# Kernel tuning notes

Hardware: AMD Instinct MI355X
Metric: run time of the kernel (lower is better)

The kernel has to match this reference:

```python
import jax, jax.numpy as jnp
import numpy as np

EPS_MASK = 1e-9   # module fills masked scores with eps, NOT -inf
LN_EPS = 1e-5

def _layer_norm(x, g, b):
    mu = jnp.mean(x, axis=-1, keepdims=True)
    var = jnp.mean(jnp.square(x - mu), axis=-1, keepdims=True)
    return (x - mu) * jax.lax.rsqrt(var + LN_EPS) * g + b

def _mha(q_in, k_in, v_in, wq, bq, wk, bk, wv, bv, wo, bo, mask, nhead):
    B, Sq, D = q_in.shape
    dk = D // nhead
    def proj(x, w, b):
        y = x @ w + b                                   # [B,S,D]
        return y.reshape(B, -1, nhead, dk).transpose(0, 2, 1, 3)  # [B,h,S,dk]
    q, k, v = proj(q_in, wq, bq), proj(k_in, wk, bk), proj(v_in, wv, bv)
    scores = jnp.einsum('bhqd,bhkd->bhqk', q, k) / np.sqrt(dk).astype(q.dtype)
    if mask is not None:
        scores = jnp.where(mask[:, None, :, :] == 0, jnp.asarray(EPS_MASK, scores.dtype), scores)
    p = jax.nn.softmax(scores, axis=-1)                 # dropout = identity (eval)
    x = jnp.einsum('bhqk,bhkd->bhqd', p, v)
    x = x.transpose(0, 2, 1, 3).reshape(B, Sq, D)
    return x @ wo + bo

def _forward_post(tgt, memory, tgt_pos, memory_pos, tgt_mask, memory_mask, p):
    nhead = 8
    # self-attention (q=k=tgt+pos, v=tgt)
    q = tgt + tgt_pos
    sa = _mha(q, q, tgt, p['sa_wq'], p['sa_bq'], p['sa_wk'], p['sa_bk'],
              p['sa_wv'], p['sa_bv'], p['sa_wo'], p['sa_bo'], tgt_mask, nhead)
    tgt = _layer_norm(tgt + sa, p['ln1_g'], p['ln1_b'])
    # cross-attention (q=tgt+tgt_pos, k=memory+memory_pos, v=memory)
    mq = tgt + tgt_pos
    mk = memory + memory_pos
    ca = _mha(mq, mk, memory, p['ca_wq'], p['ca_bq'], p['ca_wk'], p['ca_bk'],
              p['ca_wv'], p['ca_bv'], p['ca_wo'], p['ca_bo'], memory_mask, nhead)
    tgt = _layer_norm(tgt + ca, p['ln2_g'], p['ln2_b'])
    # FFN
    h = jax.nn.relu(tgt @ p['mlp_w1'] + p['mlp_b1'])
    ff = h @ p['mlp_w2'] + p['mlp_b2']
    return _layer_norm(tgt + ff, p['ln3_g'], p['ln3_b'])

def setup_inputs() -> dict:
    key = jax.random.key(0)
    B, S, M, D, H = 4, 1024, 1024, 512, 2048
    ks = iter(jax.random.split(key, 40))
    d = {
        'tgt': jax.random.normal(next(ks), (B, S, D), jnp.float32),
        'memory': jax.random.normal(next(ks), (B, M, D), jnp.float32),
        'tgt_pos': jax.random.normal(next(ks), (B, S, D), jnp.float32),
        'memory_pos': jax.random.normal(next(ks), (B, M, D), jnp.float32),
        'tgt_mask': jax.random.randint(next(ks), (B, S, S), 0, 2, jnp.int32),
        'memory_mask': jax.random.randint(next(ks), (B, S, M), 0, 2, jnp.int32),
    }
    for pre in ('sa', 'ca'):
        for nm in ('q', 'k', 'v', 'o'):
            d[f'{pre}_w{nm}'] = jax.random.normal(next(ks), (D, D), jnp.float32) * 0.02
            d[f'{pre}_b{nm}'] = jnp.zeros((D,), jnp.float32)
    for i in (1, 2, 3):
        d[f'ln{i}_g'] = jnp.ones((D,), jnp.float32)
        d[f'ln{i}_b'] = jnp.zeros((D,), jnp.float32)
    d['mlp_w1'] = jax.random.normal(next(ks), (D, H), jnp.float32) * 0.02
    d['mlp_b1'] = jnp.zeros((H,), jnp.float32)
    d['mlp_w2'] = jax.random.normal(next(ks), (H, D), jnp.float32) * 0.02
    d['mlp_b2'] = jnp.zeros((D,), jnp.float32)
    return d

def reference(tgt, memory, tgt_pos, memory_pos, tgt_mask, memory_mask,
              sa_wq, sa_bq, sa_wk, sa_bk, sa_wv, sa_bv, sa_wo, sa_bo,
              ca_wq, ca_bq, ca_wk, ca_bk, ca_wv, ca_bv, ca_wo, ca_bo,
              ln1_g, ln1_b, ln2_g, ln2_b, ln3_g, ln3_b,
              mlp_w1, mlp_b1, mlp_w2, mlp_b2):
    p = dict(sa_wq=sa_wq, sa_bq=sa_bq, sa_wk=sa_wk, sa_bk=sa_bk, sa_wv=sa_wv,
             sa_bv=sa_bv, sa_wo=sa_wo, sa_bo=sa_bo, ca_wq=ca_wq, ca_bq=ca_bq,
             ca_wk=ca_wk, ca_bk=ca_bk, ca_wv=ca_wv, ca_bv=ca_bv, ca_wo=ca_wo,
             ca_bo=ca_bo, ln1_g=ln1_g, ln1_b=ln1_b, ln2_g=ln2_g, ln2_b=ln2_b,
             ln3_g=ln3_g, ln3_b=ln3_b, mlp_w1=mlp_w1, mlp_b1=mlp_b1,
             mlp_w2=mlp_w2, mlp_b2=mlp_b2)
    return _forward_post(tgt, memory, tgt_pos, memory_pos, tgt_mask, memory_mask, p)
```

## Files before the change

### kernel.cpp

```cpp
#include <hip/hip_runtime.h>
#include <stdint.h>

typedef unsigned int u32;
typedef unsigned long long u64;
typedef unsigned short u16;
typedef __attribute__((ext_vector_type(8))) __bf16 bf16x8;
typedef __attribute__((ext_vector_type(4))) float f32x4;

#define DEV __device__ __forceinline__

DEV u16 f2bf(float f) {
    u32 x = __builtin_bit_cast(u32, f);
    u32 r = (x + 0x7FFFu + ((x >> 16) & 1u)) >> 16;
    return (u16)r;
}

DEV float bf2f(u16 x) {
    u32 u = (u32)x << 16;
    return __builtin_bit_cast(float, u);
}

DEV void unp8(uint4 u, float* f) {
    f[0] = bf2f((u16)u.x); f[1] = bf2f((u16)(u.x >> 16));
    f[2] = bf2f((u16)u.y); f[3] = bf2f((u16)(u.y >> 16));
    f[4] = bf2f((u16)u.z); f[5] = bf2f((u16)(u.z >> 16));
    f[6] = bf2f((u16)u.w); f[7] = bf2f((u16)(u.w >> 16));
}

DEV bf16x8 ldg8(const u16* p) {
    return __builtin_bit_cast(bf16x8, *(const uint4*)p);
}

DEV u32 pk2(float a, float b) {
    return (u32)f2bf(a) | ((u32)f2bf(b) << 16);
}

DEV void g2l16(const u16* g, u16* l) {
    __builtin_amdgcn_global_load_lds(
        (const __attribute__((address_space(1))) u32*)g,
        (__attribute__((address_space(3))) u32*)l, 16, 0, 0);
}

DEV f32x4 mfma16(bf16x8 a, bf16x8 b, f32x4 c) {
    return __builtin_amdgcn_mfma_f32_16x16x32_bf16(a, b, c, 0, 0, 0);
}

struct ProArgs {
    const float* w[10];
    u16* wtbase;
    const float4 *tgt, *tpos, *mem, *mpos;
    ushort4 *qin, *tgtb, *memb, *mkb, *tposb;
    const int4 *m1, *m2;
    u32 *o1, *o2;
};
__global__ __launch_bounds__(256) void prologue_kernel(ProArgs a) {
    const int bx = blockIdx.x, t = threadIdx.x;
    if (bx < 10240) {
        int z = bx >> 10, bxx = bx & 1023;
        int Kd = (z == 9) ? 2048 : 512;
        int Nd = (z == 8) ? 2048 : 512;
        size_t off = (z < 8) ? (size_t)z * 262144
                             : (z == 8 ? (size_t)2097152 : (size_t)3145728);
        u16* out = a.wtbase + off;
        int nx = Nd / 32;
        int txile = bxx % nx, tyile = bxx / nx;
        if (tyile >= Kd / 32) return;
        const float* w = a.w[z];
        __shared__ float tl[32][33];
        int tx = t & 31, ty = t >> 5;
#pragma unroll
        for (int j = 0; j < 4; ++j)
            tl[ty + j * 8][tx] = w[(size_t)(tyile * 32 + ty + j * 8) * Nd + txile * 32 + tx];
        __syncthreads();
#pragma unroll
        for (int j = 0; j < 4; ++j)
            out[(size_t)(txile * 32 + ty + j * 8) * Kd + tyile * 32 + tx] = f2bf(tl[tx][ty + j * 8]);
    } else if (bx < 12288) {
        int i = (bx - 10240) * 256 + t;
        float4 tt = a.tgt[i], p = a.tpos[i], m = a.mem[i], mp = a.mpos[i];
        a.qin[i]  = make_ushort4(f2bf(tt.x + p.x), f2bf(tt.y + p.y), f2bf(tt.z + p.z), f2bf(tt.w + p.w));
        a.tgtb[i] = make_ushort4(f2bf(tt.x), f2bf(tt.y), f2bf(tt.z), f2bf(tt.w));
        a.memb[i] = make_ushort4(f2bf(m.x), f2bf(m.y), f2bf(m.z), f2bf(m.w));
        a.mkb[i]  = make_ushort4(f2bf(m.x + mp.x), f2bf(m.y + mp.y), f2bf(m.z + mp.z), f2bf(m.w + mp.w));
        a.tposb[i]= make_ushort4(f2bf(p.x), f2bf(p.y), f2bf(p.z), f2bf(p.w));
    } else {
        int i = (bx - 12288) * 256 + t;
        const int n8 = 524288;
        bool first = i < n8;
        int idx = first ? i : i - n8;
        const int4* src = first ? a.m1 : a.m2;
        int4 x = src[idx * 2], y = src[idx * 2 + 1];
        u32 by = (u32)(x.x != 0) | ((u32)(x.y != 0) << 1) | ((u32)(x.z != 0) << 2) |
                 ((u32)(x.w != 0) << 3) | ((u32)(y.x != 0) << 4) | ((u32)(y.y != 0) << 5) |
                 ((u32)(y.z != 0) << 6) | ((u32)(y.w != 0) << 7);
        u32 w = by | (__shfl_down(by, 1) << 8) | (__shfl_down(by, 2) << 16) |
                (__shfl_down(by, 3) << 24);
        if ((t & 3) == 0) (first ? a.o1 : a.o2)[idx >> 2] = w;
    }
}

struct GemmSet { const u16* A; const u16* W; const float* bias; void* out; float oscale; int epi; };
struct GemmArgs5 { GemmSet s[5]; };

template <int BM, int BN>
__global__ __launch_bounds__(256) void gemm_kernel(GemmArgs5 args, int M, int N, int Kd) {
    constexpr int MF = BM / 32, NF = BN / 32;
    const GemmSet gs = args.s[blockIdx.z];
    const u16* __restrict__ A = gs.A;
    const u16* __restrict__ W = gs.W;
    const int t = threadIdx.x;
    const int lane = t & 63;
    const int g = lane >> 4, r16 = lane & 15;
    const int wave = t >> 6;
    const int wm = wave >> 1, wn = wave & 1;
    const int nwg = gridDim.x * gridDim.y;
    const int fid = blockIdx.y * gridDim.x + blockIdx.x;
    const int qq = nwg >> 3;
    const int lid = (fid & 7) * qq + (fid >> 3);
    const int m0 = (lid / gridDim.x) * BM, n0 = (lid % gridDim.x) * BN;

    __shared__ __align__(16) u16 As[BM * 64];
    __shared__ __align__(16) u16 Bs[BN * 64];

    f32x4 acc[MF][NF];
#pragma unroll
    for (int m = 0; m < MF; ++m)
#pragma unroll
        for (int n = 0; n < NF; ++n) acc[m][n] = f32x4{0.f, 0.f, 0.f, 0.f};

    for (int kk = 0; kk < Kd; kk += 64) {
        __syncthreads();
#pragma unroll
        for (int i = 0; i < BM / 32; ++i) {
            int cid = t + i * 256, row = cid >> 3, c = cid & 7;
            g2l16(A + (size_t)(m0 + row) * Kd + kk + ((c ^ (row & 7)) << 3), &As[cid << 3]);
        }
#pragma unroll
        for (int i = 0; i < BN / 32; ++i) {
            int cid = t + i * 256, row = cid >> 3, c = cid & 7;
            g2l16(W + (size_t)(n0 + row) * Kd + kk + ((c ^ (row & 7)) << 3), &Bs[cid << 3]);
        }
        __syncthreads();
#pragma unroll
        for (int ks = 0; ks < 2; ++ks) {
            bf16x8 af[MF], bfr[NF];
#pragma unroll
            for (int m = 0; m < MF; ++m) {
                int row = wm * (MF * 16) + m * 16 + r16;
                af[m] = *(const bf16x8*)&As[(row << 6) + (((ks * 4 + g) ^ (row & 7)) << 3)];
            }
#pragma unroll
            for (int n = 0; n < NF; ++n) {
                int row = wn * (NF * 16) + n * 16 + r16;
                bfr[n] = *(const bf16x8*)&Bs[(row << 6) + (((ks * 4 + g) ^ (row & 7)) << 3)];
            }
#pragma unroll
            for (int m = 0; m < MF; ++m)
#pragma unroll
                for (int n = 0; n < NF; ++n)
                    acc[m][n] = mfma16(af[m], bfr[n], acc[m][n]);
        }
    }
    const int epi = gs.epi;
#pragma unroll
    for (int m = 0; m < MF; ++m) {
        int row0 = m0 + wm * (MF * 16) + m * 16 + g * 4;
#pragma unroll
        for (int n = 0; n < NF; ++n) {
            int col = n0 + wn * (NF * 16) + n * 16 + r16;
            float bv = gs.bias[col];
            float v[4];
#pragma unroll
            for (int r = 0; r < 4; ++r) v[r] = (acc[m][n][r] + bv) * gs.oscale;
            if (epi == 1) {
#pragma unroll
                for (int r = 0; r < 4; ++r) v[r] = fmaxf(v[r], 0.f);
            }
            if (epi == 3) {
                int bb = row0 >> 10, s = row0 & 1023;
                u16* o = (u16*)gs.out +
                         ((size_t)(bb * 8 + (col >> 6)) * 64 + (col & 63)) * 1024 + s;
                *(ushort4*)o = make_ushort4(f2bf(v[0]), f2bf(v[1]), f2bf(v[2]), f2bf(v[3]));
            } else {
                u16* o = (u16*)gs.out;
#pragma unroll
                for (int r = 0; r < 4; ++r) o[(size_t)(row0 + r) * N + col] = f2bf(v[r]);
            }
        }
    }
}

__global__ __launch_bounds__(512) void attn_part_kernel(
    const u16* __restrict__ Q, const u16* __restrict__ K,
    const u16* __restrict__ VT, const u32* __restrict__ mb,
    u16* __restrict__ OP, float2* __restrict__ ML, int Lq, int Lk) {
    const int t = threadIdx.x, lane = t & 63, wave = t >> 6;
    const int g = lane >> 4, r16 = lane & 15;
    const int h = blockIdx.y;
    const int b = blockIdx.z >> 1, p = blockIdx.z & 1;
    const int bh = b * 8 + h;
    const int q0 = blockIdx.x * 128 + wave * 16;
    const int kc0 = p * (Lk >> 1);
    const int NCH = (Lk >> 1) >> 5;

    __shared__ __align__(16) u16 Ks[2][32][64];
    __shared__ __align__(16) u16 Vs[2][64][32];
    __shared__ __align__(16) u16 Pl[8][16][40];

    const size_t qrow = (size_t)b * Lq + q0 + r16;
    const u16* qp = Q + qrow * 512 + h * 64 + g * 8;
    bf16x8 qb0 = ldg8(qp), qb1 = ldg8(qp + 32);
    const u32* mrow = mb + qrow * (Lk >> 5);

    const int sid = t & 255;
    const bool isK = t < 256;
    const int srow = sid >> 3, sc = sid & 7;
    const int vd = sid >> 2, vc = sid & 3;
    const u16* sg = isK
        ? K + (size_t)b * Lk * 512 + h * 64 + (size_t)srow * 512 + ((sc ^ (srow & 7)) << 3)
        : VT + ((size_t)bh * 64 + vd) * Lk + (vc << 3);
    u16* const sl = (isK ? &Ks[0][0][0] : &Vs[0][0][0]) + sid * 8;
    const size_t sstride = isK ? 512 : 1;

    f32x4 acc[4];
#pragma unroll
    for (int dt = 0; dt < 4; ++dt) acc[dt] = f32x4{0.f, 0.f, 0.f, 0.f};
    float mrun = -INFINITY, lrun = 0.f;
    const f32x4 zf = {0.f, 0.f, 0.f, 0.f};

    g2l16(sg + (size_t)kc0 * sstride, sl);
    __syncthreads();

    for (int c = 0; c < NCH; ++c) {
        const int buf = c & 1, nbuf = buf ^ 1;
        const int kc = kc0 + c * 32;
        if (c + 1 < NCH)
            g2l16(sg + (size_t)(kc + 32) * sstride, sl + nbuf * 2048);
        const u16* kb = &Ks[buf][0][0];
        const u16* vb = &Vs[buf][0][0];
        const int r1 = 16 + r16;
        bf16x8 k00 = *(const bf16x8*)(kb + r16 * 64 + ((g ^ (r16 & 7)) << 3));
        bf16x8 k01 = *(const bf16x8*)(kb + r16 * 64 + (((4 + g) ^ (r16 & 7)) << 3));
        bf16x8 k10 = *(const bf16x8*)(kb + r1 * 64 + ((g ^ (r16 & 7)) << 3));
        bf16x8 k11 = *(const bf16x8*)(kb + r1 * 64 + (((4 + g) ^ (r16 & 7)) << 3));
        f32x4 s0 = mfma16(k00, qb0, zf); s0 = mfma16(k01, qb1, s0);
        f32x4 s1 = mfma16(k10, qb0, zf); s1 = mfma16(k11, qb1, s1);

        u32 mw = mrow[kc >> 5];
        float sv[8];
#pragma unroll
        for (int r = 0; r < 4; ++r) {
            sv[r]     = ((mw >> (g * 4 + r)) & 1) ? s0[r] : 1e-9f;
            sv[4 + r] = ((mw >> (16 + g * 4 + r)) & 1) ? s1[r] : 1e-9f;
        }
        float tm = fmaxf(fmaxf(fmaxf(sv[0], sv[1]), fmaxf(sv[2], sv[3])),
                         fmaxf(fmaxf(sv[4], sv[5]), fmaxf(sv[6], sv[7])));
        tm = fmaxf(tm, __shfl_xor(tm, 16));
        tm = fmaxf(tm, __shfl_xor(tm, 32));
        if (!__all(tm <= mrun + 8.f)) {
            float mn = fmaxf(mrun, tm);
            float alpha = __expf(mrun - mn);
            mrun = mn;
            lrun *= alpha;
#pragma unroll
            for (int r = 0; r < 4; ++r) {
                float ar = __shfl(alpha, g * 4 + r);
#pragma unroll
                for (int dt = 0; dt < 4; ++dt) acc[dt][r] *= ar;
            }
        }
        float ts = 0.f;
#pragma unroll
        for (int j = 0; j < 8; ++j) { sv[j] = __expf(sv[j] - mrun); ts += sv[j]; }
        ts += __shfl_xor(ts, 16);
        ts += __shfl_xor(ts, 32);
        lrun += ts;

        uint2 u0; u0.x = pk2(sv[0], sv[1]); u0.y = pk2(sv[2], sv[3]);
        uint2 u1; u1.x = pk2(sv[4], sv[5]); u1.y = pk2(sv[6], sv[7]);
        *(uint2*)&Pl[wave][r16][g * 4] = u0;
        *(uint2*)&Pl[wave][r16][16 + g * 4] = u1;
        bf16x8 pf = *(const bf16x8*)&Pl[wave][r16][g * 8];
#pragma unroll
        for (int dt = 0; dt < 4; ++dt) {
            bf16x8 vf = *(const bf16x8*)(vb + (dt * 16 + r16) * 32 + g * 8);
            acc[dt] = mfma16(pf, vf, acc[dt]);
        }
        __syncthreads();
    }

    if (lane < 16)
        ML[(size_t)p * 32768 + (size_t)bh * 1024 + q0 + lane] = make_float2(mrun, lrun);
    const size_t obase = (size_t)p * 2097152 + ((size_t)bh * 1024 + q0) * 64;
#pragma unroll
    for (int dt = 0; dt < 4; ++dt)
#pragma unroll
        for (int r = 0; r < 4; ++r)
            OP[obase + (size_t)(g * 4 + r) * 64 + dt * 16 + r16] = f2bf(acc[dt][r]);
}

__global__ __launch_bounds__(256) void attn_combine_kernel(
    const u16* __restrict__ OP, const float2* __restrict__ ML, u16* __restrict__ O) {
    int gid = blockIdx.x * 256 + threadIdx.x;
    int row = gid >> 3, seg = gid & 7;
    size_t idx = (size_t)row * 64 + seg * 8;
    float2 ml0 = ML[row], ml1 = ML[32768 + row];
    float M = fmaxf(ml0.x, ml1.x);
    float w0 = __expf(ml0.x - M), w1 = __expf(ml1.x - M);
    float rden = 1.f / (ml0.y * w0 + ml1.y * w1);
    w0 *= rden; w1 *= rden;
    float a[8], b[8];
    unp8(*(const uint4*)(OP + idx), a);
    unp8(*(const uint4*)(OP + 2097152 + idx), b);
    int bh = row >> 10, q = row & 1023;
    int bb = bh >> 3, h = bh & 7;
    u16* o = O + ((size_t)(bb * 1024 + q)) * 512 + h * 64 + seg * 8;
    uint4 r;
    r.x = pk2(a[0] * w0 + b[0] * w1, a[1] * w0 + b[1] * w1);
    r.y = pk2(a[2] * w0 + b[2] * w1, a[3] * w0 + b[3] * w1);
    r.z = pk2(a[4] * w0 + b[4] * w1, a[5] * w0 + b[5] * w1);
    r.w = pk2(a[6] * w0 + b[6] * w1, a[7] * w0 + b[7] * w1);
    *(uint4*)o = r;
}

template <int MODE>
__global__ __launch_bounds__(256) void ln_kernel(
    const u16* __restrict__ a, const u16* __restrict__ bsrc,
    const float* __restrict__ gam, const float* __restrict__ bet,
    const u16* __restrict__ pos,
    u16* __restrict__ yb, u16* __restrict__ qb, float* __restrict__ yf) {
    const int lane = threadIdx.x & 63;
    const int row = blockIdx.x * 4 + (threadIdx.x >> 6);
    const size_t base = (size_t)row * 512 + lane * 8;
    float av[8], bv[8];
    unp8(*(const uint4*)(a + base), av);
    unp8(*(const uint4*)(bsrc + base), bv);
    float x[8];
#pragma unroll
    for (int j = 0; j < 8; ++j) x[j] = av[j] + bv[j];
    float s1 = 0.f, s2 = 0.f;
#pragma unroll
    for (int j = 0; j < 8; ++j) { s1 += x[j]; s2 += x[j] * x[j]; }
#pragma unroll
    for (int d = 1; d < 64; d <<= 1) { s1 += __shfl_xor(s1, d); s2 += __shfl_xor(s2, d); }
    float mean = s1 * (1.f / 512.f);
    float var = s2 * (1.f / 512.f) - mean * mean;
    float rs = rsqrtf(var + 1e-5f);
    float4 gv0 = ((const float4*)(gam + lane * 8))[0];
    float4 gv1 = ((const float4*)(gam + lane * 8))[1];
    float4 be0 = ((const float4*)(bet + lane * 8))[0];
    float4 be1 = ((const float4*)(bet + lane * 8))[1];
    float gg[8] = {gv0.x, gv0.y, gv0.z, gv0.w, gv1.x, gv1.y, gv1.z, gv1.w};
    float bb[8] = {be0.x, be0.y, be0.z, be0.w, be1.x, be1.y, be1.z, be1.w};
    float y[8];
#pragma unroll
    for (int j = 0; j < 8; ++j) y[j] = (x[j] - mean) * rs * gg[j] + bb[j];
    if (MODE == 2) {
        ((float4*)(yf + base))[0] = make_float4(y[0], y[1], y[2], y[3]);
        ((float4*)(yf + base))[1] = make_float4(y[4], y[5], y[6], y[7]);
        return;
    }
    uint4 r;
    r.x = pk2(y[0], y[1]); r.y = pk2(y[2], y[3]);
    r.z = pk2(y[4], y[5]); r.w = pk2(y[6], y[7]);
    *(uint4*)(yb + base) = r;
    if (MODE == 0) {
        float pv[8];
        unp8(*(const uint4*)(pos + base), pv);
        uint4 q;
        q.x = pk2(y[0] + pv[0], y[1] + pv[1]);
        q.y = pk2(y[2] + pv[2], y[3] + pv[3]);
        q.z = pk2(y[4] + pv[4], y[5] + pv[5]);
        q.w = pk2(y[6] + pv[6], y[7] + pv[7]);
        *(uint4*)(qb + base) = q;
    }
}

extern "C" void kernel_launch(void* const* d_in, const int* in_sizes, int n_in,
                              void* d_out, int out_size, void* d_ws, size_t ws_size,
                              hipStream_t stream) {
    (void)in_sizes; (void)n_in; (void)out_size; (void)ws_size;
    const float* tgt      = (const float*)d_in[0];
    const float* memory   = (const float*)d_in[1];
    const float* tgt_pos  = (const float*)d_in[2];
    const float* mem_pos  = (const float*)d_in[3];
    const int*   tgt_mask = (const int*)d_in[4];
    const int*   mem_mask = (const int*)d_in[5];
    const float* sa_b[4] = {(const float*)d_in[7], (const float*)d_in[9],
                            (const float*)d_in[11], (const float*)d_in[13]};
    const float* ca_b[4] = {(const float*)d_in[15], (const float*)d_in[17],
                            (const float*)d_in[19], (const float*)d_in[21]};
    const float* ln1_g = (const float*)d_in[22]; const float* ln1_b = (const float*)d_in[23];
    const float* ln2_g = (const float*)d_in[24]; const float* ln2_b = (const float*)d_in[25];
    const float* ln3_g = (const float*)d_in[26]; const float* ln3_b = (const float*)d_in[27];
    const float* mlp_b1 = (const float*)d_in[29];
    const float* mlp_b2 = (const float*)d_in[31];

    const size_t MiB = 1024 * 1024;
    char* ws = (char*)d_ws;
    u16*  WT  = (u16*)(ws + 0);
    u32*  MBS = (u32*)(ws + 8 * MiB);
    u32*  MBC = (u32*)(ws + 8 * MiB + 512 * 1024);
    u16*  QIN = (u16*)(ws + 9 * MiB);
    u16*  TGTB= (u16*)(ws + 13 * MiB);
    u16*  MEMB= (u16*)(ws + 17 * MiB);
    u16*  MKB = (u16*)(ws + 21 * MiB);
    u16*  QM  = (u16*)(ws + 25 * MiB);
    u16*  KMS = (u16*)(ws + 29 * MiB);
    u16*  KMC = (u16*)(ws + 33 * MiB);
    u16*  VTS = (u16*)(ws + 37 * MiB);
    u16*  VTC = (u16*)(ws + 41 * MiB);
    u16*  ATNB= (u16*)(ws + 45 * MiB);
    u16*  PROJB = (u16*)(ws + 49 * MiB);
    u16*  X1B = (u16*)(ws + 53 * MiB);
    u16*  MQB = (u16*)(ws + 57 * MiB);
    u16*  X2B = (u16*)(ws + 61 * MiB);
    u16*  TPB = (u16*)(ws + 65 * MiB);
    u16*  FFH = (u16*)(ws + 9 * MiB);
    u16*  OPB = (u16*)(ws + 96 * MiB);
    float2* MLB = (float2*)(ws + 120 * MiB);

    u16* wt[10];
    for (int z = 0; z < 8; ++z) wt[z] = WT + (size_t)z * 262144;
    wt[8] = WT + 2097152;
    wt[9] = WT + 3145728;

    ProArgs pa;
    pa.w[0] = (const float*)d_in[6];  pa.w[1] = (const float*)d_in[8];
    pa.w[2] = (const float*)d_in[10]; pa.w[3] = (const float*)d_in[12];
    pa.w[4] = (const float*)d_in[14]; pa.w[5] = (const float*)d_in[16];
    pa.w[6] = (const float*)d_in[18]; pa.w[7] = (const float*)d_in[20];
    pa.w[8] = (const float*)d_in[28]; pa.w[9] = (const float*)d_in[30];
    pa.wtbase = WT;
    pa.tgt = (const float4*)tgt; pa.tpos = (const float4*)tgt_pos;
    pa.mem = (const float4*)memory; pa.mpos = (const float4*)mem_pos;
    pa.qin = (ushort4*)QIN; pa.tgtb = (ushort4*)TGTB;
    pa.memb = (ushort4*)MEMB; pa.mkb = (ushort4*)MKB;
    pa.tposb = (ushort4*)TPB;
    pa.m1 = (const int4*)tgt_mask; pa.m2 = (const int4*)mem_mask;
    pa.o1 = MBS; pa.o2 = MBC;
    prologue_kernel<<<16384, 256, 0, stream>>>(pa);

    GemmArgs5 ga;
    ga.s[0] = {QIN,  wt[0], sa_b[0], QM,  0.125f, 0};
    ga.s[1] = {QIN,  wt[1], sa_b[1], KMS, 1.f,    0};
    ga.s[2] = {TGTB, wt[2], sa_b[2], VTS, 1.f,    3};
    ga.s[3] = {MKB,  wt[5], ca_b[1], KMC, 1.f,    0};
    ga.s[4] = {MEMB, wt[6], ca_b[2], VTC, 1.f,    3};
    gemm_kernel<128, 64><<<dim3(8, 32, 5), 256, 0, stream>>>(ga, 4096, 512, 512);
    attn_part_kernel<<<dim3(8, 8, 8), 512, 0, stream>>>(QM, KMS, VTS, MBS, OPB, MLB, 1024, 1024);
    attn_combine_kernel<<<1024, 256, 0, stream>>>(OPB, MLB, ATNB);
    ga.s[0] = {ATNB, wt[3], sa_b[3], PROJB, 1.f, 0};
    ga.s[1] = ga.s[0]; ga.s[2] = ga.s[0]; ga.s[3] = ga.s[0]; ga.s[4] = ga.s[0];
    gemm_kernel<64, 64><<<dim3(8, 64, 1), 256, 0, stream>>>(ga, 4096, 512, 512);
    ln_kernel<0><<<1024, 256, 0, stream>>>(TGTB, PROJB, ln1_g, ln1_b, TPB, X1B, MQB, nullptr);

    ga.s[0] = {MQB, wt[4], ca_b[0], QM, 0.125f, 0};
    ga.s[1] = ga.s[0]; ga.s[2] = ga.s[0]; ga.s[3] = ga.s[0]; ga.s[4] = ga.s[0];
    gemm_kernel<128, 64><<<dim3(8, 32, 1), 256, 0, stream>>>(ga, 4096, 512, 512);
    attn_part_kernel<<<dim3(8, 8, 8), 512, 0, stream>>>(QM, KMC, VTC, MBC, OPB, MLB, 1024, 1024);
    attn_combine_kernel<<<1024, 256, 0, stream>>>(OPB, MLB, ATNB);
    ga.s[0] = {ATNB, wt[7], ca_b[3], PROJB, 1.f, 0};
    ga.s[1] = ga.s[0]; ga.s[2] = ga.s[0]; ga.s[3] = ga.s[0]; ga.s[4] = ga.s[0];
    gemm_kernel<64, 64><<<dim3(8, 64, 1), 256, 0, stream>>>(ga, 4096, 512, 512);
    ln_kernel<1><<<1024, 256, 0, stream>>>(X1B, PROJB, ln2_g, ln2_b, nullptr, X2B, nullptr, nullptr);

    ga.s[0] = {X2B, wt[8], mlp_b1, FFH, 1.f, 1};
    ga.s[1] = ga.s[0]; ga.s[2] = ga.s[0]; ga.s[3] = ga.s[0]; ga.s[4] = ga.s[0];
    gemm_kernel<128, 64><<<dim3(32, 32, 1), 256, 0, stream>>>(ga, 4096, 2048, 512);
    ga.s[0] = {FFH, wt[9], mlp_b2, PROJB, 1.f, 0};
    ga.s[1] = ga.s[0]; ga.s[2] = ga.s[0]; ga.s[3] = ga.s[0]; ga.s[4] = ga.s[0];
    gemm_kernel<64, 64><<<dim3(8, 64, 1), 256, 0, stream>>>(ga, 4096, 512, 2048);
    ln_kernel<2><<<1024, 256, 0, stream>>>(X2B, PROJB, ln3_g, ln3_b, nullptr,
                                           nullptr, nullptr, (float*)d_out);
}
```

Before: 177.7 us.

## Split-K the N=512 projection GEMMs and sum partials in layernorm

The three output-projection GEMMs (self-attn out, cross-attn out, FFN down) now split K in two across blockIdx.z, writing two bf16 partial outputs. The residual layernorm kernels read both partials and add them, which doubles the number of workgroups for these otherwise under-filled 512-wide GEMMs. The cross-attention Q projection also switches from 128x64 to 64x64 tiles for more blocks. The cost is an extra bf16 round trip per partial, extra bf16 rounding of partial sums, and more memory traffic in layernorm.

```diff
diff --git a/kernel.cpp b/kernel.cpp
--- a/kernel.cpp
+++ b/kernel.cpp
@@ -99,7 +99,10 @@
     }
 }
 
-struct GemmSet { const u16* A; const u16* W; const float* bias; void* out; float oscale; int epi; };
+struct GemmSet {
+    const u16* A; const u16* W; const float* bias; void* out;
+    float oscale; int epi; int k0; int klen;
+};
 struct GemmArgs5 { GemmSet s[5]; };
 
 template <int BM, int BN>
@@ -128,7 +131,8 @@
 #pragma unroll
         for (int n = 0; n < NF; ++n) acc[m][n] = f32x4{0.f, 0.f, 0.f, 0.f};
 
-    for (int kk = 0; kk < Kd; kk += 64) {
+    const int kend = gs.k0 + gs.klen;
+    for (int kk = gs.k0; kk < kend; kk += 64) {
         __syncthreads();
 #pragma unroll
         for (int i = 0; i < BM / 32; ++i) {
@@ -168,7 +172,7 @@
 #pragma unroll
         for (int n = 0; n < NF; ++n) {
             int col = n0 + wn * (NF * 16) + n * 16 + r16;
-            float bv = gs.bias[col];
+            float bv = gs.bias ? gs.bias[col] : 0.f;
             float v[4];
 #pragma unroll
             for (int r = 0; r < 4; ++r) v[r] = (acc[m][n][r] + bv) * gs.oscale;
@@ -325,19 +329,20 @@
 
 template <int MODE>
 __global__ __launch_bounds__(256) void ln_kernel(
-    const u16* __restrict__ a, const u16* __restrict__ bsrc,
+    const u16* __restrict__ a, const u16* __restrict__ b1, const u16* __restrict__ b2,
     const float* __restrict__ gam, const float* __restrict__ bet,
     const u16* __restrict__ pos,
     u16* __restrict__ yb, u16* __restrict__ qb, float* __restrict__ yf) {
     const int lane = threadIdx.x & 63;
     const int row = blockIdx.x * 4 + (threadIdx.x >> 6);
     const size_t base = (size_t)row * 512 + lane * 8;
-    float av[8], bv[8];
+    float av[8], bv[8], cv[8];
     unp8(*(const uint4*)(a + base), av);
-    unp8(*(const uint4*)(bsrc + base), bv);
+    unp8(*(const uint4*)(b1 + base), bv);
+    unp8(*(const uint4*)(b2 + base), cv);
     float x[8];
 #pragma unroll
-    for (int j = 0; j < 8; ++j) x[j] = av[j] + bv[j];
+    for (int j = 0; j < 8; ++j) x[j] = av[j] + bv[j] + cv[j];
     float s1 = 0.f, s2 = 0.f;
 #pragma unroll
     for (int j = 0; j < 8; ++j) { s1 += x[j]; s2 += x[j] * x[j]; }
@@ -411,7 +416,8 @@
     u16*  VTS = (u16*)(ws + 37 * MiB);
     u16*  VTC = (u16*)(ws + 41 * MiB);
     u16*  ATNB= (u16*)(ws + 45 * MiB);
-    u16*  PROJB = (u16*)(ws + 49 * MiB);
+    u16*  P1B = (u16*)(ws + 49 * MiB);
+    u16*  P2B = (u16*)(ws + 69 * MiB);
     u16*  X1B = (u16*)(ws + 53 * MiB);
     u16*  MQB = (u16*)(ws + 57 * MiB);
     u16*  X2B = (u16*)(ws + 61 * MiB);
@@ -442,35 +448,38 @@
     prologue_kernel<<<16384, 256, 0, stream>>>(pa);
 
     GemmArgs5 ga;
-    ga.s[0] = {QIN,  wt[0], sa_b[0], QM,  0.125f, 0};
-    ga.s[1] = {QIN,  wt[1], sa_b[1], KMS, 1.f,    0};
-    ga.s[2] = {TGTB, wt[2], sa_b[2], VTS, 1.f,    3};
-    ga.s[3] = {MKB,  wt[5], ca_b[1], KMC, 1.f,    0};
-    ga.s[4] = {MEMB, wt[6], ca_b[2], VTC, 1.f,    3};
+    ga.s[0] = {QIN,  wt[0], sa_b[0], QM,  0.125f, 0, 0, 512};
+    ga.s[1] = {QIN,  wt[1], sa_b[1], KMS, 1.f,    0, 0, 512};
+    ga.s[2] = {TGTB, wt[2], sa_b[2], VTS, 1.f,    3, 0, 512};
+    ga.s[3] = {MKB,  wt[5], ca_b[1], KMC, 1.f,    0, 0, 512};
+    ga.s[4] = {MEMB, wt[6], ca_b[2], VTC, 1.f,    3, 0, 512};
     gemm_kernel<128, 64><<<dim3(8, 32, 5), 256, 0, stream>>>(ga, 4096, 512, 512);
     attn_part_kernel<<<dim3(8, 8, 8), 512, 0, stream>>>(QM, KMS, VTS, MBS, OPB, MLB, 1024, 1024);
     attn_combine_kernel<<<1024, 256, 0, stream>>>(OPB, MLB, ATNB);
-    ga.s[0] = {ATNB, wt[3], sa_b[3], PROJB, 1.f, 0};
+    ga.s[0] = {ATNB, wt[3], sa_b[3], P1B, 1.f, 0, 0,   256};
+    ga.s[1] = {ATNB, wt[3], nullptr, P2B, 1.f, 0, 256, 256};
+    ga.s[2] = ga.s[0]; ga.s[3] = ga.s[0]; ga.s[4] = ga.s[0];
+    gemm_kernel<64, 64><<<dim3(8, 64, 2), 256, 0, stream>>>(ga, 4096, 512, 512);
+    ln_kernel<0><<<1024, 256, 0, stream>>>(TGTB, P1B, P2B, ln1_g, ln1_b, TPB, X1B, MQB, nullptr);
+
+    ga.s[0] = {MQB, wt[4], ca_b[0], QM, 0.125f, 0, 0, 512};
     ga.s[1] = ga.s[0]; ga.s[2] = ga.s[0]; ga.s[3] = ga.s[0]; ga.s[4] = ga.s[0];
     gemm_kernel<64, 64><<<dim3(8, 64, 1), 256, 0, stream>>>(ga, 4096, 512, 512);
-    ln_kernel<0><<<1024, 256, 0, stream>>>(TGTB, PROJB, ln1_g, ln1_b, TPB, X1B, MQB, nullptr);
-
-    ga.s[0] = {MQB, wt[4], ca_b[0], QM, 0.125f, 0};
-    ga.s[1] = ga.s[0]; ga.s[2] = ga.s[0]; ga.s[3] = ga.s[0]; ga.s[4] = ga.s[0];
-    gemm_kernel<128, 64><<<dim3(8, 32, 1), 256, 0, stream>>>(ga, 4096, 512, 512);
     attn_part_kernel<<<dim3(8, 8, 8), 512, 0, stream>>>(QM, KMC, VTC, MBC, OPB, MLB, 1024, 1024);
     attn_combine_kernel<<<1024, 256, 0, stream>>>(OPB, MLB, ATNB);
-    ga.s[0] = {ATNB, wt[7], ca_b[3], PROJB, 1.f, 0};
-    ga.s[1] = ga.s[0]; ga.s[2] = ga.s[0]; ga.s[3] = ga.s[0]; ga.s[4] = ga.s[0];
-    gemm_kernel<64, 64><<<dim3(8, 64, 1), 256, 0, stream>>>(ga, 4096, 512, 512);
-    ln_kernel<1><<<1024, 256, 0, stream>>>(X1B, PROJB, ln2_g, ln2_b, nullptr, X2B, nullptr, nullptr);
-
-    ga.s[0] = {X2B, wt[8], mlp_b1, FFH, 1.f, 1};
+    ga.s[0] = {ATNB, wt[7], ca_b[3], P1B, 1.f, 0, 0,   256};
+    ga.s[1] = {ATNB, wt[7], nullptr, P2B, 1.f, 0, 256, 256};
+    ga.s[2] = ga.s[0]; ga.s[3] = ga.s[0]; ga.s[4] = ga.s[0];
+    gemm_kernel<64, 64><<<dim3(8, 64, 2), 256, 0, stream>>>(ga, 4096, 512, 512);
+    ln_kernel<1><<<1024, 256, 0, stream>>>(X1B, P1B, P2B, ln2_g, ln2_b, nullptr, X2B, nullptr, nullptr);
+
+    ga.s[0] = {X2B, wt[8], mlp_b1, FFH, 1.f, 1, 0, 512};
     ga.s[1] = ga.s[0]; ga.s[2] = ga.s[0]; ga.s[3] = ga.s[0]; ga.s[4] = ga.s[0];
     gemm_kernel<128, 64><<<dim3(32, 32, 1), 256, 0, stream>>>(ga, 4096, 2048, 512);
-    ga.s[0] = {FFH, wt[9], mlp_b2, PROJB, 1.f, 0};
-    ga.s[1] = ga.s[0]; ga.s[2] = ga.s[0]; ga.s[3] = ga.s[0]; ga.s[4] = ga.s[0];
-    gemm_kernel<64, 64><<<dim3(8, 64, 1), 256, 0, stream>>>(ga, 4096, 512, 2048);
-    ln_kernel<2><<<1024, 256, 0, stream>>>(X2B, PROJB, ln3_g, ln3_b, nullptr,
+    ga.s[0] = {FFH, wt[9], mlp_b2, P1B, 1.f, 0, 0,    1024};
+    ga.s[1] = {FFH, wt[9], nullptr, P2B, 1.f, 0, 1024, 1024};
+    ga.s[2] = ga.s[0]; ga.s[3] = ga.s[0]; ga.s[4] = ga.s[0];
+    gemm_kernel<64, 64><<<dim3(8, 64, 2), 256, 0, stream>>>(ga, 4096, 512, 2048);
+    ln_kernel<2><<<1024, 256, 0, stream>>>(X2B, P1B, P2B, ln3_g, ln3_b, nullptr,
                                            nullptr, nullptr, (float*)d_out);
 }
```

New measurement: 169.3 us. 4.7% less time.
